# Kernel tuning notes

Hardware: AMD Instinct MI355X
Metric: run time of the kernel (lower is better)

## Reference

```python
import jax, jax.numpy as jnp
import numpy as np

EPS = 1e-5
NEG_SLOPE = 0.01  # torch LeakyReLU default


def setup_inputs() -> dict:
    key = jax.random.key(0)
    k1, k2, k3, k4 = jax.random.split(key, 4)
    B, d, N, K = 8, 3, 32768, 16
    C_in, C_out = 10, 32  # rel_pos_dim, d_out // 2
    xyz_t = jax.random.normal(k1, (B, d, N), dtype=jnp.float32)
    neighbor_idx = jax.random.randint(k2, (B, N, K), 0, N, dtype=jnp.int64)
    # Conv1d(10, 32, kernel_size=1) params
    W = jax.random.normal(k3, (C_out, C_in), dtype=jnp.float32) * 0.1
    b = jnp.zeros((C_out,), dtype=jnp.float32)
    # BatchNorm1d(32) affine params
    gamma = jnp.ones((C_out,), dtype=jnp.float32)
    beta = jnp.zeros((C_out,), dtype=jnp.float32)
    return {"xyz_t": xyz_t, "neighbor_idx": neighbor_idx, "W": W, "b": b,
            "gamma": gamma, "beta": beta}


def _loc_se(xyz_t, neighbor_idx, W, b, gamma, beta):
    B, d, N = xyz_t.shape
    K = neighbor_idx.shape[-1]
    # gather neighbor coords -> [B, d, N*K]
    idx_flat = neighbor_idx.reshape(B, 1, N * K)
    neighbor_xyz = jnp.take_along_axis(xyz_t, idx_flat, axis=2)
    # each center point repeated K times consecutively -> [B, d, N*K]
    center = jnp.repeat(xyz_t, K, axis=2)
    rel = center - neighbor_xyz
    dist = jnp.sqrt(jnp.sum(rel * rel, axis=1, keepdims=True))  # [B, 1, N*K]
    feat = jnp.concatenate([dist, rel, center, neighbor_xyz], axis=1)  # [B, 10, N*K]
    # pointwise conv (1x1) 10 -> 32
    h = jnp.einsum('oc,bcl->bol', W, feat) + b[None, :, None]
    # BatchNorm1d, training-mode batch statistics over (B, L)
    mean = jnp.mean(h, axis=(0, 2), keepdims=True)
    var = jnp.mean(jnp.square(h - mean), axis=(0, 2), keepdims=True)
    y = (h - mean) / jnp.sqrt(var + EPS) * gamma[None, :, None] + beta[None, :, None]
    # LeakyReLU
    return jnp.where(y >= 0, y, NEG_SLOPE * y)


def reference(xyz_t, neighbor_idx, W, b, gamma, beta):
    return _loc_se(xyz_t, neighbor_idx, W, b, gamma, beta)
```

## Files before the change

### kernel.cpp

```cpp
#include <hip/hip_runtime.h>
#include <math.h>

#define BB 8
#define NN 32768
#define KK 16
#define NP (BB * NN)
#define LL (NN * KK)
#define NG 26
#define NC 9
#define NBLKT 1024
#define NBLKS 1024
#define NSPB 8192
#define MS (BB * NSPB * KK)
#define EPSV 1e-5

#define CHP 2048
#define CHQ 512
#define NCHB 256

#define XYZP_OFF 0
#define GPART_OFF (NP * 16)
#define CPART_OFF (GPART_OFF + NBLKS * NG * 4)
#define FW_OFF    (CPART_OFF + NBLKT * NC * 4)

typedef float nfloat4 __attribute__((ext_vector_type(4)));

__device__ __forceinline__ float bf4(float x) {
    x += __shfl_xor(x, 4, 64);
    x += __shfl_xor(x, 8, 64);
    x += __shfl_xor(x, 16, 64);
    x += __shfl_xor(x, 32, 64);
    return x;
}

__global__ __launch_bounds__(256) void k_transpose(const float* __restrict__ xyz,
                                                   float4* __restrict__ xyzp,
                                                   float* __restrict__ cpart) {
    int t = blockIdx.x * 256 + threadIdx.x;
    int b = t >> 15;
    int n = t & (NN - 1);
    const float* p = xyz + (size_t)b * 3 * NN + n;
    float x = p[0], y = p[NN], z = p[2 * NN];
    xyzp[t] = make_float4(x, y, z, 0.0f);

    float cv[NC] = {x, y, z, x * x, x * y, x * z, y * y, y * z, z * z};
#pragma unroll
    for (int j = 0; j < NC; ++j) cv[j] = bf4(cv[j]);

    __shared__ float red[16][NC + 1];
    int wave = threadIdx.x >> 6;
    int lane = threadIdx.x & 63;
    if (lane < 4) {
#pragma unroll
        for (int j = 0; j < NC; ++j) red[wave * 4 + lane][j] = cv[j];
    }
    __syncthreads();
    if (threadIdx.x < NC) {
        int j = threadIdx.x;
        float s = 0.f;
#pragma unroll
        for (int r = 0; r < 16; ++r) s += red[r][j];
        cpart[(size_t)blockIdx.x * NC + j] = s;
    }
}

__global__ __launch_bounds__(256) void k_stats(const float4* __restrict__ xyzp,
                                               const int4* __restrict__ idx4,
                                               float* __restrict__ gpart) {
    int s = blockIdx.x * 256 + threadIdx.x;
    int b = s >> 15;
    int u = s & 32767;
    int n = u >> 2;
    int q = u & 3;
    int pbase = b << 15;
    int pt = pbase + n;
    float4 c = xyzp[pt];

    float sd = 0.f, sd2 = 0.f;
    float sg0 = 0.f, sg1 = 0.f, sg2 = 0.f;
    float sdg0 = 0.f, sdg1 = 0.f, sdg2 = 0.f;
    float s00 = 0.f, s01 = 0.f, s02 = 0.f, s11 = 0.f, s12 = 0.f, s22 = 0.f;

    int4 iv = idx4[(size_t)pt * 4 + q];
    int ids[4] = {iv.x, iv.y, iv.z, iv.w};
#pragma unroll
    for (int j = 0; j < 4; ++j) {
        float4 g = xyzp[pbase + ids[j]];
        float r0 = c.x - g.x, r1 = c.y - g.y, r2 = c.z - g.z;
        float d2 = r0 * r0 + r1 * r1 + r2 * r2;
        float d  = sqrtf(d2);
        sd += d;  sd2 += d2;
        sg0 += g.x; sg1 += g.y; sg2 += g.z;
        sdg0 += d * g.x; sdg1 += d * g.y; sdg2 += d * g.z;
        s00 += g.x * g.x; s01 += g.x * g.y; s02 += g.x * g.z;
        s11 += g.y * g.y; s12 += g.y * g.z; s22 += g.z * g.z;
    }

    float gv[NG];
    gv[0] = sd;
    gv[1] = sg0;  gv[2] = sg1;  gv[3] = sg2;
    gv[4] = sd2;
    gv[5] = c.x * sd;  gv[6] = c.y * sd;  gv[7] = c.z * sd;
    gv[8] = sdg0; gv[9] = sdg1; gv[10] = sdg2;
    gv[11] = c.x * sg0; gv[12] = c.x * sg1; gv[13] = c.x * sg2;
    gv[14] = c.y * sg0; gv[15] = c.y * sg1; gv[16] = c.y * sg2;
    gv[17] = c.z * sg0; gv[18] = c.z * sg1; gv[19] = c.z * sg2;
    gv[20] = s00; gv[21] = s01; gv[22] = s02;
    gv[23] = s11; gv[24] = s12; gv[25] = s22;

#pragma unroll
    for (int j = 0; j < NG; ++j) gv[j] = bf4(gv[j]);

    __shared__ float red[16][NG + 1];
    int wave = threadIdx.x >> 6;
    int lane = threadIdx.x & 63;
    if (lane < 4) {
#pragma unroll
        for (int j = 0; j < NG; ++j) red[wave * 4 + lane][j] = gv[j];
    }
    __syncthreads();
    if (threadIdx.x < NG) {
        int j = threadIdx.x;
        float ss = 0.f;
#pragma unroll
        for (int r = 0; r < 16; ++r) ss += red[r][j];
        gpart[(size_t)blockIdx.x * NG + j] = ss;
    }
}

__global__ void k_finalize(const float* __restrict__ gpart,
                           const float* __restrict__ cpart,
                           const float* __restrict__ W,
                           const float* __restrict__ bias,
                           const float* __restrict__ gamma,
                           const float* __restrict__ beta,
                           float* __restrict__ fw) {
    __shared__ double part[8][35];
    int j  = threadIdx.x;
    int cy = threadIdx.y;
    double s = 0.0;
    if (j < NG) {
        for (int i = cy * 128; i < (cy + 1) * 128; ++i)
            s += (double)gpart[(size_t)i * NG + j];
    } else {
        int jc = j - NG;
        for (int i = cy * 128; i < (cy + 1) * 128; ++i)
            s += (double)cpart[(size_t)i * NC + jc];
    }
    part[cy][j] = s;
    __syncthreads();

    __shared__ double G[NG], C[NC];
    if (cy == 0) {
        double tot = 0.0;
        for (int y = 0; y < 8; ++y) tot += part[y][j];
        if (j < NG) G[j] = tot; else C[j - NG] = tot;
    }
    __syncthreads();

    int tid = cy * 35 + j;
    if (tid < 32) {
        int o = tid;
        double M[7];
        M[0] = (double)W[o * 10 + 0];
        for (int x = 0; x < 3; ++x) {
            M[1 + x] = (double)W[o * 10 + 1 + x] + (double)W[o * 10 + 4 + x];
            M[4 + x] = (double)W[o * 10 + 7 + x] - (double)W[o * 10 + 1 + x];
        }
        const double invS = 1.0 / (double)MS;
        const double invP = 1.0 / (double)NP;

        double mf[7];
        mf[0] = G[0] * invS;
        mf[1] = C[0] * invP; mf[2] = C[1] * invP; mf[3] = C[2] * invP;
        mf[4] = G[1] * invS; mf[5] = G[2] * invS; mf[6] = G[3] * invS;

        double S2[28];
        S2[0]  = G[4]  * invS;
        S2[1]  = G[5]  * invS;  S2[2]  = G[6]  * invS;  S2[3]  = G[7]  * invS;
        S2[4]  = G[8]  * invS;  S2[5]  = G[9]  * invS;  S2[6]  = G[10] * invS;
        S2[7]  = C[3]  * invP;  S2[8]  = C[4]  * invP;  S2[9]  = C[5]  * invP;
        S2[10] = G[11] * invS;  S2[11] = G[12] * invS;  S2[12] = G[13] * invS;
        S2[13] = C[6]  * invP;  S2[14] = C[7]  * invP;
        S2[15] = G[14] * invS;  S2[16] = G[15] * invS;  S2[17] = G[16] * invS;
        S2[18] = C[8]  * invP;
        S2[19] = G[17] * invS;  S2[20] = G[18] * invS;  S2[21] = G[19] * invS;
        S2[22] = G[20] * invS;  S2[23] = G[21] * invS;  S2[24] = G[22] * invS;
        S2[25] = G[23] * invS;  S2[26] = G[24] * invS;
        S2[27] = G[25] * invS;

        double mh = (double)bias[o];
        for (int i = 0; i < 7; ++i) mh += M[i] * mf[i];
        double var = 0.0;
        for (int i = 0; i < 7; ++i)
            for (int k = 0; k < 7; ++k) {
                int a = i < k ? i : k;
                int b2 = i < k ? k : i;
                int u = 7 * a - (a * (a - 1)) / 2 + (b2 - a);
                double cov = S2[u] - mf[i] * mf[k];
                var += M[i] * M[k] * cov;
            }
        double sc = (double)gamma[o] / sqrt(var + EPSV);
        for (int x = 0; x < 7; ++x) fw[o * 8 + x] = (float)(M[x] * sc);
        fw[o * 8 + 7] = (float)(((double)bias[o] - mh) * sc + (double)beta[o]);
    }
}

__global__ __launch_bounds__(256) void k_apply_v2(const float4* __restrict__ xyzp,
                                                  const int4* __restrict__ idx4,
                                                  const float* __restrict__ fw,
                                                  float* __restrict__ out) {
    __shared__ float sdl[CHP], sgx[CHP], sgy[CHP], sgz[CHP];
    int bid = blockIdx.x;
    int b   = bid >> 8;
    int ch  = bid & (NCHB - 1);
    int tid = threadIdx.x;
    int pbase = b << 15;
    size_t qglob = (size_t)bid * CHQ;

#pragma unroll
    for (int it = 0; it < 2; ++it) {
        int q  = it * 256 + tid;
        int qb = ch * CHQ + q;
        int4 iv = idx4[qglob + q];
        float4 c = xyzp[pbase + (qb >> 2)];
        int ids[4] = {iv.x, iv.y, iv.z, iv.w};
        float dv[4], gxv[4], gyv[4], gzv[4];
#pragma unroll
        for (int j = 0; j < 4; ++j) {
            float4 g = xyzp[pbase + ids[j]];
            float r0 = c.x - g.x, r1 = c.y - g.y, r2 = c.z - g.z;
            dv[j]  = sqrtf(r0 * r0 + r1 * r1 + r2 * r2);
            gxv[j] = g.x; gyv[j] = g.y; gzv[j] = g.z;
        }
        *(float4*)&sdl[q * 4] = make_float4(dv[0], dv[1], dv[2], dv[3]);
        *(float4*)&sgx[q * 4] = make_float4(gxv[0], gxv[1], gxv[2], gxv[3]);
        *(float4*)&sgy[q * 4] = make_float4(gyv[0], gyv[1], gyv[2], gyv[3]);
        *(float4*)&sgz[q * 4] = make_float4(gzv[0], gzv[1], gzv[2], gzv[3]);
    }
    __syncthreads();

    float4 c0 = xyzp[pbase + ((ch * CHQ + tid) >> 2)];
    float4 c1 = xyzp[pbase + ((ch * CHQ + 256 + tid) >> 2)];

    const float4* fw4 = (const float4*)fw;
    float* ob = out + (size_t)b * 32 * LL + (size_t)ch * CHP;
#pragma unroll 4
    for (int oi = 0; oi < 32; ++oi) {
        int o = (oi + bid) & 31;
        float4 wA = fw4[o * 2];
        float4 wB = fw4[o * 2 + 1];
        float* oo = ob + (size_t)o * LL;
#pragma unroll
        for (int it2 = 0; it2 < 2; ++it2) {
            int q2 = it2 * 256 + tid;
            float4 c = it2 ? c1 : c0;
            float hc = wB.w + wA.y * c.x + wA.z * c.y + wA.w * c.z;
            float4 d4 = *(const float4*)&sdl[q2 * 4];
            float4 x4 = *(const float4*)&sgx[q2 * 4];
            float4 y4 = *(const float4*)&sgy[q2 * 4];
            float4 z4 = *(const float4*)&sgz[q2 * 4];
            float h0 = hc + wA.x * d4.x + wB.x * x4.x + wB.y * y4.x + wB.z * z4.x;
            float h1 = hc + wA.x * d4.y + wB.x * x4.y + wB.y * y4.y + wB.z * z4.y;
            float h2 = hc + wA.x * d4.z + wB.x * x4.z + wB.y * y4.z + wB.z * z4.z;
            float h3 = hc + wA.x * d4.w + wB.x * x4.w + wB.y * y4.w + wB.z * z4.w;
            nfloat4 r = {fmaxf(h0, 0.01f * h0), fmaxf(h1, 0.01f * h1),
                         fmaxf(h2, 0.01f * h2), fmaxf(h3, 0.01f * h3)};
            __builtin_nontemporal_store(r, (nfloat4*)(oo + q2 * 4));
        }
    }
}

extern "C" void kernel_launch(void* const* d_in, const int* in_sizes, int n_in,
                              void* d_out, int out_size, void* d_ws, size_t ws_size,
                              hipStream_t stream) {
    const float* xyz   = (const float*)d_in[0];
    const int*   nidx  = (const int*)d_in[1];
    const float* W     = (const float*)d_in[2];
    const float* bias  = (const float*)d_in[3];
    const float* gamma = (const float*)d_in[4];
    const float* beta  = (const float*)d_in[5];
    float*       out   = (float*)d_out;

    char* ws = (char*)d_ws;
    float4* xyzp  = (float4*)(ws + XYZP_OFF);
    float*  gpart = (float*)(ws + GPART_OFF);
    float*  cpart = (float*)(ws + CPART_OFF);
    float*  fw    = (float*)(ws + FW_OFF);
    const int4* idx4 = (const int4*)nidx;

    k_transpose<<<NBLKT, 256, 0, stream>>>(xyz, xyzp, cpart);
    k_stats<<<NBLKS, 256, 0, stream>>>(xyzp, idx4, gpart);
    k_finalize<<<1, dim3(35, 8), 0, stream>>>(gpart, cpart, W, bias, gamma, beta, fw);
    k_apply_v2<<<BB * NCHB, 256, 0, stream>>>(xyzp, idx4, fw, out);
}
```

Measured before the change: 142.3 us.

## Fuse finalize into stats via last-block atomic and keep apply data in registers

The single-block finalize kernel is folded into the stats kernel. A global atomic counter, reset in the transpose kernel, picks the last finishing block, which then reduces the partial sums and computes the folded weights. This removes one kernel launch and its gap. The apply kernel also drops its shared-memory staging and barrier, keeping gathered distances and coordinates in registers, which raises register pressure.

```diff
diff --git a/kernel.cpp b/kernel.cpp
--- a/kernel.cpp
+++ b/kernel.cpp
@@ -22,6 +22,7 @@
 #define GPART_OFF (NP * 16)
 #define CPART_OFF (GPART_OFF + NBLKS * NG * 4)
 #define FW_OFF    (CPART_OFF + NBLKT * NC * 4)
+#define CNT_OFF   (FW_OFF + 1024)
 
 typedef float nfloat4 __attribute__((ext_vector_type(4)));
 
@@ -35,8 +36,10 @@
 
 __global__ __launch_bounds__(256) void k_transpose(const float* __restrict__ xyz,
                                                    float4* __restrict__ xyzp,
-                                                   float* __restrict__ cpart) {
+                                                   float* __restrict__ cpart,
+                                                   unsigned int* __restrict__ cnt) {
     int t = blockIdx.x * 256 + threadIdx.x;
+    if (t == 0) *cnt = 0u;
     int b = t >> 15;
     int n = t & (NN - 1);
     const float* p = xyz + (size_t)b * 3 * NN + n;
@@ -66,7 +69,14 @@
 
 __global__ __launch_bounds__(256) void k_stats(const float4* __restrict__ xyzp,
                                                const int4* __restrict__ idx4,
-                                               float* __restrict__ gpart) {
+                                               float* __restrict__ gpart,
+                                               const float* __restrict__ cpart,
+                                               const float* __restrict__ W,
+                                               const float* __restrict__ bias,
+                                               const float* __restrict__ gamma,
+                                               const float* __restrict__ beta,
+                                               float* __restrict__ fw,
+                                               unsigned int* __restrict__ cnt) {
     int s = blockIdx.x * 256 + threadIdx.x;
     int b = s >> 15;
     int u = s & 32767;
@@ -126,41 +136,42 @@
         for (int r = 0; r < 16; ++r) ss += red[r][j];
         gpart[(size_t)blockIdx.x * NG + j] = ss;
     }
-}
-
-__global__ void k_finalize(const float* __restrict__ gpart,
-                           const float* __restrict__ cpart,
-                           const float* __restrict__ W,
-                           const float* __restrict__ bias,
-                           const float* __restrict__ gamma,
-                           const float* __restrict__ beta,
-                           float* __restrict__ fw) {
+
+    __threadfence();
+    __shared__ unsigned int isLast;
+    if (threadIdx.x == 0)
+        isLast = (atomicAdd(cnt, 1u) == NBLKS - 1) ? 1u : 0u;
+    __syncthreads();
+    if (!isLast) return;
+    __threadfence();
+
     __shared__ double part[8][35];
-    int j  = threadIdx.x;
-    int cy = threadIdx.y;
-    double s = 0.0;
-    if (j < NG) {
-        for (int i = cy * 128; i < (cy + 1) * 128; ++i)
-            s += (double)gpart[(size_t)i * NG + j];
-    } else {
-        int jc = j - NG;
-        for (int i = cy * 128; i < (cy + 1) * 128; ++i)
-            s += (double)cpart[(size_t)i * NC + jc];
-    }
-    part[cy][j] = s;
+    for (int idx = threadIdx.x; idx < 280; idx += 256) {
+        int cy = idx / 35, j = idx % 35;
+        double sum = 0.0;
+        if (j < NG) {
+            for (int i = cy * 128; i < (cy + 1) * 128; ++i)
+                sum += (double)gpart[(size_t)i * NG + j];
+        } else {
+            int jc = j - NG;
+            for (int i = cy * 128; i < (cy + 1) * 128; ++i)
+                sum += (double)cpart[(size_t)i * NC + jc];
+        }
+        part[cy][j] = sum;
+    }
     __syncthreads();
 
     __shared__ double G[NG], C[NC];
-    if (cy == 0) {
+    if (threadIdx.x < 35) {
+        int j = threadIdx.x;
         double tot = 0.0;
         for (int y = 0; y < 8; ++y) tot += part[y][j];
         if (j < NG) G[j] = tot; else C[j - NG] = tot;
     }
     __syncthreads();
 
-    int tid = cy * 35 + j;
-    if (tid < 32) {
-        int o = tid;
+    if (threadIdx.x < 32) {
+        int o = threadIdx.x;
         double M[7];
         M[0] = (double)W[o * 10 + 0];
         for (int x = 0; x < 3; ++x) {
@@ -196,8 +207,8 @@
             for (int k = 0; k < 7; ++k) {
                 int a = i < k ? i : k;
                 int b2 = i < k ? k : i;
-                int u = 7 * a - (a * (a - 1)) / 2 + (b2 - a);
-                double cov = S2[u] - mf[i] * mf[k];
+                int uu = 7 * a - (a * (a - 1)) / 2 + (b2 - a);
+                double cov = S2[uu] - mf[i] * mf[k];
                 var += M[i] * M[k] * cov;
             }
         double sc = (double)gamma[o] / sqrt(var + EPSV);
@@ -206,11 +217,10 @@
     }
 }
 
-__global__ __launch_bounds__(256) void k_apply_v2(const float4* __restrict__ xyzp,
+__global__ __launch_bounds__(256) void k_apply_v3(const float4* __restrict__ xyzp,
                                                   const int4* __restrict__ idx4,
                                                   const float* __restrict__ fw,
                                                   float* __restrict__ out) {
-    __shared__ float sdl[CHP], sgx[CHP], sgy[CHP], sgz[CHP];
     int bid = blockIdx.x;
     int b   = bid >> 8;
     int ch  = bid & (NCHB - 1);
@@ -218,12 +228,13 @@
     int pbase = b << 15;
     size_t qglob = (size_t)bid * CHQ;
 
+    float4 cs[2], d4[2], x4[2], y4[2], z4[2];
 #pragma unroll
     for (int it = 0; it < 2; ++it) {
-        int q  = it * 256 + tid;
-        int qb = ch * CHQ + q;
+        int q = it * 256 + tid;
         int4 iv = idx4[qglob + q];
-        float4 c = xyzp[pbase + (qb >> 2)];
+        float4 c = xyzp[pbase + ((ch * CHQ + q) >> 2)];
+        cs[it] = c;
         int ids[4] = {iv.x, iv.y, iv.z, iv.w};
         float dv[4], gxv[4], gyv[4], gzv[4];
 #pragma unroll
@@ -233,15 +244,11 @@
             dv[j]  = sqrtf(r0 * r0 + r1 * r1 + r2 * r2);
             gxv[j] = g.x; gyv[j] = g.y; gzv[j] = g.z;
         }
-        *(float4*)&sdl[q * 4] = make_float4(dv[0], dv[1], dv[2], dv[3]);
-        *(float4*)&sgx[q * 4] = make_float4(gxv[0], gxv[1], gxv[2], gxv[3]);
-        *(float4*)&sgy[q * 4] = make_float4(gyv[0], gyv[1], gyv[2], gyv[3]);
-        *(float4*)&sgz[q * 4] = make_float4(gzv[0], gzv[1], gzv[2], gzv[3]);
-    }
-    __syncthreads();
-
-    float4 c0 = xyzp[pbase + ((ch * CHQ + tid) >> 2)];
-    float4 c1 = xyzp[pbase + ((ch * CHQ + 256 + tid) >> 2)];
+        d4[it] = make_float4(dv[0], dv[1], dv[2], dv[3]);
+        x4[it] = make_float4(gxv[0], gxv[1], gxv[2], gxv[3]);
+        y4[it] = make_float4(gyv[0], gyv[1], gyv[2], gyv[3]);
+        z4[it] = make_float4(gzv[0], gzv[1], gzv[2], gzv[3]);
+    }
 
     const float4* fw4 = (const float4*)fw;
     float* ob = out + (size_t)b * 32 * LL + (size_t)ch * CHP;
@@ -252,18 +259,13 @@
         float4 wB = fw4[o * 2 + 1];
         float* oo = ob + (size_t)o * LL;
 #pragma unroll
-        for (int it2 = 0; it2 < 2; ++it2) {
-            int q2 = it2 * 256 + tid;
-            float4 c = it2 ? c1 : c0;
-            float hc = wB.w + wA.y * c.x + wA.z * c.y + wA.w * c.z;
-            float4 d4 = *(const float4*)&sdl[q2 * 4];
-            float4 x4 = *(const float4*)&sgx[q2 * 4];
-            float4 y4 = *(const float4*)&sgy[q2 * 4];
-            float4 z4 = *(const float4*)&sgz[q2 * 4];
-            float h0 = hc + wA.x * d4.x + wB.x * x4.x + wB.y * y4.x + wB.z * z4.x;
-            float h1 = hc + wA.x * d4.y + wB.x * x4.y + wB.y * y4.y + wB.z * z4.y;
-            float h2 = hc + wA.x * d4.z + wB.x * x4.z + wB.y * y4.z + wB.z * z4.z;
-            float h3 = hc + wA.x * d4.w + wB.x * x4.w + wB.y * y4.w + wB.z * z4.w;
+        for (int it = 0; it < 2; ++it) {
+            int q2 = it * 256 + tid;
+            float hc = wB.w + wA.y * cs[it].x + wA.z * cs[it].y + wA.w * cs[it].z;
+            float h0 = hc + wA.x * d4[it].x + wB.x * x4[it].x + wB.y * y4[it].x + wB.z * z4[it].x;
+            float h1 = hc + wA.x * d4[it].y + wB.x * x4[it].y + wB.y * y4[it].y + wB.z * z4[it].y;
+            float h2 = hc + wA.x * d4[it].z + wB.x * x4[it].z + wB.y * y4[it].z + wB.z * z4[it].z;
+            float h3 = hc + wA.x * d4[it].w + wB.x * x4[it].w + wB.y * y4[it].w + wB.z * z4[it].w;
             nfloat4 r = {fmaxf(h0, 0.01f * h0), fmaxf(h1, 0.01f * h1),
                          fmaxf(h2, 0.01f * h2), fmaxf(h3, 0.01f * h3)};
             __builtin_nontemporal_store(r, (nfloat4*)(oo + q2 * 4));
@@ -287,10 +289,11 @@
     float*  gpart = (float*)(ws + GPART_OFF);
     float*  cpart = (float*)(ws + CPART_OFF);
     float*  fw    = (float*)(ws + FW_OFF);
+    unsigned int* cnt = (unsigned int*)(ws + CNT_OFF);
     const int4* idx4 = (const int4*)nidx;
 
-    k_transpose<<<NBLKT, 256, 0, stream>>>(xyz, xyzp, cpart);
-    k_stats<<<NBLKS, 256, 0, stream>>>(xyzp, idx4, gpart);
-    k_finalize<<<1, dim3(35, 8), 0, stream>>>(gpart, cpart, W, bias, gamma, beta, fw);
-    k_apply_v2<<<BB * NCHB, 256, 0, stream>>>(xyzp, idx4, fw, out);
-}
+    k_transpose<<<NBLKT, 256, 0, stream>>>(xyz, xyzp, cpart, cnt);
+    k_stats<<<NBLKS, 256, 0, stream>>>(xyzp, idx4, gpart, cpart,
+                                       W, bias, gamma, beta, fw, cnt);
+    k_apply_v3<<<BB * NCHB, 256, 0, stream>>>(xyzp, idx4, fw, out);
+}
```

New measurement: 218.0 us. +53.2%, slower.

## Process two chunks per block and prefetch second chunk's gathers during first write-out

Applied to the files above, without the earlier changes.

The apply kernel now handles two consecutive chunks per block, halving the grid. The neighbor-index and gathered-coordinate loads for the second chunk are issued into registers before the first chunk's 32-channel output loop, so their latency overlaps the output stores. The cost is higher register pressure from holding 10 float4 values per thread, which may lower occupancy, and fewer blocks to spread across CUs.

```diff
diff --git a/kernel.cpp b/kernel.cpp
--- a/kernel.cpp
+++ b/kernel.cpp
@@ -6,6 +6,7 @@
 #define KK 16
 #define NP (BB * NN)
 #define LL (NN * KK)
+#define QPB (LL / 4)
 #define NG 26
 #define NC 9
 #define NBLKT 1024
@@ -16,7 +17,6 @@
 
 #define CHP 2048
 #define CHQ 512
-#define NCHB 256
 
 #define XYZP_OFF 0
 #define GPART_OFF (NP * 16)
@@ -206,24 +206,27 @@
     }
 }
 
-__global__ __launch_bounds__(256) void k_apply_v2(const float4* __restrict__ xyzp,
+__global__ __launch_bounds__(256) void k_apply_v4(const float4* __restrict__ xyzp,
                                                   const int4* __restrict__ idx4,
                                                   const float* __restrict__ fw,
                                                   float* __restrict__ out) {
     __shared__ float sdl[CHP], sgx[CHP], sgy[CHP], sgz[CHP];
     int bid = blockIdx.x;
-    int b   = bid >> 8;
-    int ch  = bid & (NCHB - 1);
+    int b   = bid >> 7;
+    int cp  = bid & 127;
     int tid = threadIdx.x;
     int pbase = b << 15;
-    size_t qglob = (size_t)bid * CHQ;
+    int ch0 = cp * 2;
+    int ch1 = ch0 + 1;
+    size_t qb0 = (size_t)b * QPB + (size_t)ch0 * CHQ;
+    size_t qb1 = qb0 + CHQ;
+    const float4* fw4 = (const float4*)fw;
 
 #pragma unroll
     for (int it = 0; it < 2; ++it) {
         int q  = it * 256 + tid;
-        int qb = ch * CHQ + q;
-        int4 iv = idx4[qglob + q];
-        float4 c = xyzp[pbase + (qb >> 2)];
+        int4 iv = idx4[qb0 + q];
+        float4 c = xyzp[pbase + ((ch0 * CHQ + q) >> 2)];
         int ids[4] = {iv.x, iv.y, iv.z, iv.w};
         float dv[4], gxv[4], gyv[4], gzv[4];
 #pragma unroll
@@ -238,23 +241,33 @@
         *(float4*)&sgy[q * 4] = make_float4(gyv[0], gyv[1], gyv[2], gyv[3]);
         *(float4*)&sgz[q * 4] = make_float4(gzv[0], gzv[1], gzv[2], gzv[3]);
     }
-    __syncthreads();
-
-    float4 c0 = xyzp[pbase + ((ch * CHQ + tid) >> 2)];
-    float4 c1 = xyzp[pbase + ((ch * CHQ + 256 + tid) >> 2)];
-
-    const float4* fw4 = (const float4*)fw;
-    float* ob = out + (size_t)b * 32 * LL + (size_t)ch * CHP;
+    float4 c00 = xyzp[pbase + ((ch0 * CHQ + tid) >> 2)];
+    float4 c01 = xyzp[pbase + ((ch0 * CHQ + 256 + tid) >> 2)];
+    __syncthreads();
+
+    float4 cs1[2], g1[2][4];
+#pragma unroll
+    for (int it = 0; it < 2; ++it) {
+        int q = it * 256 + tid;
+        int4 iv = idx4[qb1 + q];
+        cs1[it] = xyzp[pbase + ((ch1 * CHQ + q) >> 2)];
+        int ids[4] = {iv.x, iv.y, iv.z, iv.w};
+#pragma unroll
+        for (int j = 0; j < 4; ++j)
+            g1[it][j] = xyzp[pbase + ids[j]];
+    }
+
+    float* ob0 = out + (size_t)b * 32 * LL + (size_t)ch0 * CHP;
 #pragma unroll 4
     for (int oi = 0; oi < 32; ++oi) {
         int o = (oi + bid) & 31;
         float4 wA = fw4[o * 2];
         float4 wB = fw4[o * 2 + 1];
-        float* oo = ob + (size_t)o * LL;
+        float* oo = ob0 + (size_t)o * LL;
 #pragma unroll
         for (int it2 = 0; it2 < 2; ++it2) {
             int q2 = it2 * 256 + tid;
-            float4 c = it2 ? c1 : c0;
+            float4 c = it2 ? c01 : c00;
             float hc = wB.w + wA.y * c.x + wA.z * c.y + wA.w * c.z;
             float4 d4 = *(const float4*)&sdl[q2 * 4];
             float4 x4 = *(const float4*)&sgx[q2 * 4];
@@ -269,6 +282,52 @@
             __builtin_nontemporal_store(r, (nfloat4*)(oo + q2 * 4));
         }
     }
+    __syncthreads();
+
+#pragma unroll
+    for (int it = 0; it < 2; ++it) {
+        int q = it * 256 + tid;
+        float4 c = cs1[it];
+        float dv[4], gxv[4], gyv[4], gzv[4];
+#pragma unroll
+        for (int j = 0; j < 4; ++j) {
+            float4 g = g1[it][j];
+            float r0 = c.x - g.x, r1 = c.y - g.y, r2 = c.z - g.z;
+            dv[j]  = sqrtf(r0 * r0 + r1 * r1 + r2 * r2);
+            gxv[j] = g.x; gyv[j] = g.y; gzv[j] = g.z;
+        }
+        *(float4*)&sdl[q * 4] = make_float4(dv[0], dv[1], dv[2], dv[3]);
+        *(float4*)&sgx[q * 4] = make_float4(gxv[0], gxv[1], gxv[2], gxv[3]);
+        *(float4*)&sgy[q * 4] = make_float4(gyv[0], gyv[1], gyv[2], gyv[3]);
+        *(float4*)&sgz[q * 4] = make_float4(gzv[0], gzv[1], gzv[2], gzv[3]);
+    }
+    __syncthreads();
+
+    float* ob1 = out + (size_t)b * 32 * LL + (size_t)ch1 * CHP;
+#pragma unroll 4
+    for (int oi = 0; oi < 32; ++oi) {
+        int o = (oi + bid) & 31;
+        float4 wA = fw4[o * 2];
+        float4 wB = fw4[o * 2 + 1];
+        float* oo = ob1 + (size_t)o * LL;
+#pragma unroll
+        for (int it2 = 0; it2 < 2; ++it2) {
+            int q2 = it2 * 256 + tid;
+            float4 c = cs1[it2];
+            float hc = wB.w + wA.y * c.x + wA.z * c.y + wA.w * c.z;
+            float4 d4 = *(const float4*)&sdl[q2 * 4];
+            float4 x4 = *(const float4*)&sgx[q2 * 4];
+            float4 y4 = *(const float4*)&sgy[q2 * 4];
+            float4 z4 = *(const float4*)&sgz[q2 * 4];
+            float h0 = hc + wA.x * d4.x + wB.x * x4.x + wB.y * y4.x + wB.z * z4.x;
+            float h1 = hc + wA.x * d4.y + wB.x * x4.y + wB.y * y4.y + wB.z * z4.y;
+            float h2 = hc + wA.x * d4.z + wB.x * x4.z + wB.y * y4.z + wB.z * z4.z;
+            float h3 = hc + wA.x * d4.w + wB.x * x4.w + wB.y * y4.w + wB.z * z4.w;
+            nfloat4 r = {fmaxf(h0, 0.01f * h0), fmaxf(h1, 0.01f * h1),
+                         fmaxf(h2, 0.01f * h2), fmaxf(h3, 0.01f * h3)};
+            __builtin_nontemporal_store(r, (nfloat4*)(oo + q2 * 4));
+        }
+    }
 }
 
 extern "C" void kernel_launch(void* const* d_in, const int* in_sizes, int n_in,
@@ -292,5 +351,5 @@
     k_transpose<<<NBLKT, 256, 0, stream>>>(xyz, xyzp, cpart);
     k_stats<<<NBLKS, 256, 0, stream>>>(xyzp, idx4, gpart);
     k_finalize<<<1, dim3(35, 8), 0, stream>>>(gpart, cpart, W, bias, gamma, beta, fw);
-    k_apply_v2<<<BB * NCHB, 256, 0, stream>>>(xyzp, idx4, fw, out);
-}
+    k_apply_v4<<<BB * 128, 256, 0, stream>>>(xyzp, idx4, fw, out);
+}
```

Result: slower. 158.9 us (+11.7%).
